# Kernel optimization log

Hardware: AMD Instinct MI355X
Metric: run time of the kernel (lower is better)

Reference implementation:

```python
import jax, jax.numpy as jnp
import numpy as np

HEADS = 16
DIM_HEAD = 64
QUERY_DIM = 1024
CONTEXT_DIM = 1024
D_ATTN = HEADS * DIM_HEAD
SCALE = DIM_HEAD ** -0.5


def setup_inputs() -> dict:
    key = jax.random.key(0)
    ks = jax.random.split(key, 7)
    B, N, M = 4, 2048, 1024
    x = jax.random.normal(ks[0], (B, N, QUERY_DIM), dtype=jnp.float32)
    context = jax.random.normal(ks[1], (B, M, CONTEXT_DIM), dtype=jnp.float32)
    # Linear weights stored as [in, out] (no bias for Q/K/V, bias for to_out)
    s = 0.02
    Wq = jax.random.normal(ks[2], (QUERY_DIM, D_ATTN), dtype=jnp.float32) * s
    Wk = jax.random.normal(ks[3], (CONTEXT_DIM, D_ATTN), dtype=jnp.float32) * s
    Wv = jax.random.normal(ks[4], (CONTEXT_DIM, D_ATTN), dtype=jnp.float32) * s
    Wo = jax.random.normal(ks[5], (D_ATTN, QUERY_DIM), dtype=jnp.float32) * s
    bo = jax.random.normal(ks[6], (QUERY_DIM,), dtype=jnp.float32) * s
    return {"x": x, "context": context, "Wq": Wq, "Wk": Wk, "Wv": Wv, "Wo": Wo, "bo": bo}


def reference(x, context, Wq, Wk, Wv, Wo, bo):
    B, N, _ = x.shape
    M = context.shape[1]
    Q = (x @ Wq).reshape(B, N, HEADS, DIM_HEAD)        # b n h d
    K = (context @ Wk).reshape(B, M, HEADS, DIM_HEAD)  # b m h d
    V = (context @ Wv).reshape(B, M, HEADS, DIM_HEAD)
    # scores: b q h m  (matches torch einsum 'bqhd,bhmd->bqhm')
    scores = jnp.einsum('bqhd,bmhd->bqhm', Q, K) * SCALE
    attn = jax.nn.softmax(scores, axis=-1)
    out = jnp.einsum('bqhm,bmhd->bqhd', attn, V)
    out = out.reshape(B, N, D_ATTN)
    return out @ Wo + bo  # dropout p=0.0 -> identity
```

## Files before the change

### kernel.cpp

```cpp
#include <hip/hip_runtime.h>
#include <math.h>


#define HEADS 16
#define DHEAD 64
#define DM    1024
#define BQ    4
#define NQ    2048
#define MK    1024

typedef unsigned short u16;
typedef __attribute__((ext_vector_type(8))) short bf16x8;
typedef __attribute__((ext_vector_type(4))) float f32x4;
typedef __attribute__((ext_vector_type(16))) float f32x16;

__device__ __forceinline__ u16 f2bf(float f) {
  unsigned u = __builtin_bit_cast(unsigned, f);
  u = u + 0x7FFFu + ((u >> 16) & 1u);
  return (u16)(u >> 16);
}

__device__ __forceinline__ unsigned cvtpk(float lo, float hi2) {
  unsigned r;
  asm("v_cvt_pk_bf16_f32 %0, %1, %2" : "=v"(r) : "v"(lo), "v"(hi2));
  return r;
}

__device__ __forceinline__ float max3f(float a, float b, float c) {
  float d;
  asm("v_max3_f32 %0, %1, %2, %3" : "=v"(d) : "v"(a), "v"(b), "v"(c));
  return d;
}

__device__ __forceinline__ void gld16(const u16* g, u16* l) {
  __builtin_amdgcn_global_load_lds((const __attribute__((address_space(1))) void*)g,
                                   (__attribute__((address_space(3))) void*)l,
                                   16, 0, 0);
}

__global__ void k_cvt(const float* __restrict__ in, u16* __restrict__ out, int n8) {
  int i = blockIdx.x * 256 + threadIdx.x;
  if (i >= n8) return;
  float4 a = ((const float4*)in)[i * 2];
  float4 b = ((const float4*)in)[i * 2 + 1];
  union { u16 h[8]; int4 v; } r;
  r.h[0] = f2bf(a.x); r.h[1] = f2bf(a.y); r.h[2] = f2bf(a.z); r.h[3] = f2bf(a.w);
  r.h[4] = f2bf(b.x); r.h[5] = f2bf(b.y); r.h[6] = f2bf(b.z); r.h[7] = f2bf(b.w);
  ((int4*)out)[i] = r.v;
}

__global__ void k_wt(const float* __restrict__ W0, const float* __restrict__ W1,
                     const float* __restrict__ W2, const float* __restrict__ W3,
                     u16* __restrict__ out) {
  __shared__ float t[32][33];
  const float* W = blockIdx.z == 0 ? W0 : blockIdx.z == 1 ? W1 : blockIdx.z == 2 ? W2 : W3;
  u16* o = out + (size_t)blockIdx.z * DM * DM;
  int r0 = blockIdx.y * 32, c0 = blockIdx.x * 32;
  int tx = threadIdx.x, ty = threadIdx.y;
  for (int i = ty; i < 32; i += 8) t[i][tx] = W[(size_t)(r0 + i) * DM + c0 + tx];
  __syncthreads();
  for (int i = ty; i < 32; i += 8) o[(size_t)(c0 + i) * DM + r0 + tx] = f2bf(t[tx][i]);
}


#define STG2(buf, k0) do {                               \
  gld16(gA0 + (k0), &As[buf][w * 512]);                  \
  gld16(gA1 + (k0), &As[buf][4096 + w * 512]);           \
  gld16(gB0 + (k0), &Bs[buf][w * 512]);                  \
} while (0)

#define GEMM2_COMPUTE(cur) do {                                                          \
  bf16x8 af[4], bfr[4];                                                                  \
  _Pragma("unroll")                                                                      \
  for (int mi = 0; mi < 4; mi++)                                                         \
    af[mi]  = *(const bf16x8*)&As[cur][(wr * 64 + mi * 16 + lrow) * 32 + sl];            \
  _Pragma("unroll")                                                                      \
  for (int ni = 0; ni < 4; ni++)                                                         \
    bfr[ni] = *(const bf16x8*)&Bs[cur][(wc * 64 + ni * 16 + lrow) * 32 + sl];            \
  __builtin_amdgcn_s_setprio(1);                                                         \
  _Pragma("unroll")                                                                      \
  for (int mi = 0; mi < 4; mi++)                                                         \
    _Pragma("unroll")                                                                    \
    for (int ni = 0; ni < 4; ni++)                                                       \
      acc[mi][ni] = __builtin_amdgcn_mfma_f32_16x16x32_bf16(af[mi], bfr[ni],             \
                                                            acc[mi][ni], 0, 0, 0);      \
  __builtin_amdgcn_s_setprio(0);                                                         \
} while (0)

#define GEMM2_LOOP() do {                                      \
  STG2(0, 0);                                                  \
  _Pragma("unroll 2")                                          \
  for (int kt = 0; kt < 32; ++kt) {                            \
    int cur = kt & 1;                                          \
    if (kt < 31) {                                             \
      STG2(cur ^ 1, (kt + 1) * 32);                            \
      asm volatile("s_waitcnt vmcnt(3)" ::: "memory");         \
    } else {                                                   \
      asm volatile("s_waitcnt vmcnt(0)" ::: "memory");         \
    }                                                          \
    __builtin_amdgcn_s_barrier();                              \
    __builtin_amdgcn_sched_barrier(0);                         \
    GEMM2_COMPUTE(cur);                                        \
    __builtin_amdgcn_sched_barrier(0);                         \
    __builtin_amdgcn_s_barrier();                              \
    __builtin_amdgcn_sched_barrier(0);                         \
  }                                                            \
} while (0)

__global__ __launch_bounds__(512, 2) void k_gemm_qkv(const u16* __restrict__ xb,
                                                     const u16* __restrict__ cb,
                                                     const u16* __restrict__ wt,
                                                     u16* __restrict__ Qb,
                                                     u16* __restrict__ Kb,
                                                     u16* __restrict__ Vtb) {
  __shared__ u16 As[2][8192];
  __shared__ u16 Bs[2][4096];
  int lin = blockIdx.x;
  int swz = (lin & 7) * 64 + (lin >> 3);
  int p = swz >> 3, bx = swz & 7;
  const u16* A; const u16* Bt; u16* obf; int row0, mode;
  if (p < 32)      { A = xb; Bt = wt;           obf = Qb;  row0 = p * 256;        mode = 0; }
  else if (p < 48) { A = cb; Bt = wt + 1048576; obf = Kb;  row0 = (p - 32) * 256; mode = 0; }
  else             { A = cb; Bt = wt + 2097152; obf = Vtb; row0 = (p - 48) * 256; mode = 1; }
  int col0 = bx * 128;
  int t = threadIdx.x;
  int w = t >> 6, lane = t & 63, lrow = lane & 15, lgrp = lane >> 4;
  int wr = w >> 1, wc = w & 1;
  int sl = (lgrp ^ (lrow & 3)) * 8;
  f32x4 acc[4][4] = {};
  int srow = t >> 2;
  int scol = ((t & 3) ^ (srow & 3)) * 8;
  const u16* gA0 = A  + (size_t)(row0 + srow) * DM + scol;
  const u16* gA1 = gA0 + (size_t)128 * DM;
  const u16* gB0 = Bt + (size_t)(col0 + srow) * DM + scol;

  GEMM2_LOOP();

  #pragma unroll
  for (int mi = 0; mi < 4; mi++)
    #pragma unroll
    for (int ni = 0; ni < 4; ni++)
      #pragma unroll
      for (int j = 0; j < 4; j++) {
        int gr = row0 + wr * 64 + mi * 16 + lgrp * 4 + j;
        int gc = col0 + wc * 64 + ni * 16 + lrow;
        float v = acc[mi][ni][j];
        if (mode == 0) {
          obf[(size_t)gr * DM + gc] = f2bf(v);
        } else {
          int b = gr >> 10, m = gr & 1023;
          obf[((size_t)(b * DM + gc)) * MK + m] = f2bf(v);
        }
      }
}

__global__ __launch_bounds__(512, 2) void k_gemm_o(const u16* __restrict__ A,
                                                   const u16* __restrict__ Bt,
                                                   float* __restrict__ of32,
                                                   const float* __restrict__ bias) {
  __shared__ u16 As[2][8192];
  __shared__ u16 Bs[2][4096];
  int lin = blockIdx.x;
  int swz = (lin & 7) * 32 + (lin >> 3);
  int p = swz >> 3, bx = swz & 7;
  int row0 = p * 256, col0 = bx * 128;
  int t = threadIdx.x;
  int w = t >> 6, lane = t & 63, lrow = lane & 15, lgrp = lane >> 4;
  int wr = w >> 1, wc = w & 1;
  int sl = (lgrp ^ (lrow & 3)) * 8;
  f32x4 acc[4][4] = {};
  int srow = t >> 2;
  int scol = ((t & 3) ^ (srow & 3)) * 8;
  const u16* gA0 = A  + (size_t)(row0 + srow) * DM + scol;
  const u16* gA1 = gA0 + (size_t)128 * DM;
  const u16* gB0 = Bt + (size_t)(col0 + srow) * DM + scol;

  GEMM2_LOOP();

  #pragma unroll
  for (int mi = 0; mi < 4; mi++)
    #pragma unroll
    for (int ni = 0; ni < 4; ni++)
      #pragma unroll
      for (int j = 0; j < 4; j++) {
        int gr = row0 + wr * 64 + mi * 16 + lgrp * 4 + j;
        int gc = col0 + wc * 64 + ni * 16 + lrow;
        of32[(size_t)gr * DM + gc] = acc[mi][ni][j] + bias[gc];
      }
}

#define BUILD_PFRAG(sv, base, frag) {                     \
  unsigned a_ = cvtpk(sv[base + 0], sv[base + 1]);        \
  unsigned c_ = cvtpk(sv[base + 2], sv[base + 3]);        \
  unsigned b_ = cvtpk(sv[base + 4], sv[base + 5]);        \
  unsigned d_ = cvtpk(sv[base + 6], sv[base + 7]);        \
  asm("v_permlane32_swap_b32 %0, %1" : "+v"(a_), "+v"(b_)); \
  asm("v_permlane32_swap_b32 %0, %1" : "+v"(c_), "+v"(d_)); \
  union { unsigned w[4]; bf16x8 v; } u_;                  \
  u_.w[0] = a_;  u_.w[1] = c_;                            \
  u_.w[2] = b_;  u_.w[3] = d_;                            \
  frag = u_.v; }

#define PV_CHUNK(sv, base, c) {                                               \
  bf16x8 pf_; BUILD_PFRAG(sv, base, pf_);                                     \
  int mo_ = ((c) * 16 + hi * 8) ^ sw;                                         \
  bf16x8 vf0_ = *(const bf16x8*)&Vlc[ln * 64 + mo_];                          \
  bf16x8 vf1_ = *(const bf16x8*)&Vlc[(32 + ln) * 64 + mo_];                   \
  __builtin_amdgcn_s_setprio(1);                                              \
  o0 = __builtin_amdgcn_mfma_f32_32x32x16_bf16(vf0_, pf_, o0, 0, 0, 0);       \
  o1 = __builtin_amdgcn_mfma_f32_32x32x16_bf16(vf1_, pf_, o1, 0, 0, 0);       \
  __builtin_amdgcn_s_setprio(0); }

__device__ __forceinline__ float max16(const f32x16 &v) {
  float m0 = max3f(v[0], v[1], v[2]);
  float m1 = max3f(v[3], v[4], v[5]);
  float m2 = max3f(v[6], v[7], v[8]);
  float m3 = max3f(v[9], v[10], v[11]);
  float m4 = max3f(v[12], v[13], v[14]);
  float a = max3f(m0, m1, m2);
  float b = max3f(m3, m4, v[15]);
  return fmaxf(a, b);
}

__device__ __forceinline__ float sum16(const f32x16 &v) {
  float a = (v[0] + v[1]) + (v[2] + v[3]);
  float b = (v[4] + v[5]) + (v[6] + v[7]);
  float c = (v[8] + v[9]) + (v[10] + v[11]);
  float d = (v[12] + v[13]) + (v[14] + v[15]);
  return (a + b) + (c + d);
}

__global__ __launch_bounds__(512) void k_attn(const u16* __restrict__ Q,
                                              const u16* __restrict__ K,
                                              const u16* __restrict__ Vt,
                                              u16* __restrict__ O) {
  __shared__ __align__(16) u16 Kl[2][4096];
  __shared__ __align__(16) u16 Vl[2][4096];
  int bh = blockIdx.y, b = bh >> 4, h = bh & 15;
  int n0 = blockIdx.x * 256;
  int t = threadIdx.x, w = t >> 6, lane = t & 63;
  int ln = lane & 31, hi = lane >> 5;
  const float s2 = 0.18033688011112042f;

  int qrow = n0 + w * 32 + ln;
  const u16* qp = &Q[(((size_t)(b * NQ + qrow)) * HEADS + h) * DHEAD + hi * 8];
  bf16x8 qf0 = *(const bf16x8*)(qp);
  bf16x8 qf1 = *(const bf16x8*)(qp + 16);
  bf16x8 qf2 = *(const bf16x8*)(qp + 32);
  bf16x8 qf3 = *(const bf16x8*)(qp + 48);

  f32x16 o0 = {}, o1 = {};
  float M_ = -1e30f, L_ = 0.f;

  int srow = t >> 3, sp = (t & 7) * 8;
  const u16* kg = &K[(((size_t)(b * MK + srow)) * HEADS + h) * DHEAD + sp];
  const u16* vg = &Vt[((size_t)(b * DM) + h * DHEAD + srow) * MK + sp];
  int sd = srow * 64 + (sp ^ ((srow & 7) << 3));
  int sw = (ln & 7) << 3;

  int4 kv = *(const int4*)kg;
  int4 vv = *(const int4*)vg;
  *(int4*)&Kl[0][sd] = kv;
  *(int4*)&Vl[0][sd] = vv;
  __syncthreads();

  for (int it = 0; it < 16; ++it) {
    int cur = it & 1;
    const u16* Klc = Kl[cur];
    const u16* Vlc = Vl[cur];
    if (it < 15) {
      kv = *(const int4*)(kg + (size_t)(it + 1) * (64 * HEADS * DHEAD));
      vv = *(const int4*)(vg + (it + 1) * 64);
    }

    f32x16 s0 = {}, s1 = {};
    __builtin_amdgcn_s_setprio(1);
    #pragma unroll
    for (int kd = 0; kd < 4; ++kd) {
      int doff = (kd * 16 + hi * 8) ^ sw;
      bf16x8 kf0 = *(const bf16x8*)&Klc[ln * 64 + doff];
      bf16x8 kf1 = *(const bf16x8*)&Klc[(32 + ln) * 64 + doff];
      bf16x8 qk = kd == 0 ? qf0 : kd == 1 ? qf1 : kd == 2 ? qf2 : qf3;
      s0 = __builtin_amdgcn_mfma_f32_32x32x16_bf16(kf0, qk, s0, 0, 0, 0);
      s1 = __builtin_amdgcn_mfma_f32_32x32x16_bf16(kf1, qk, s1, 0, 0, 0);
    }
    __builtin_amdgcn_s_setprio(0);

    float vm = fmaxf(max16(s0), max16(s1));

    if (!__all(vm - M_ <= 8.0f)) {
      float vm2 = fmaxf(vm, __shfl_xor(vm, 32));
      float mn = fmaxf(M_, vm2);
      float rc = exp2f((M_ - mn) * s2);
      M_ = mn;
      L_ *= rc;
      #pragma unroll
      for (int i = 0; i < 16; ++i) { o0[i] *= rc; o1[i] *= rc; }
    }
    float nb = M_ * s2;
    #pragma unroll
    for (int i = 0; i < 16; ++i) s0[i] = exp2f(s0[i] * s2 - nb);
    #pragma unroll
    for (int i = 0; i < 16; ++i) s1[i] = exp2f(s1[i] * s2 - nb);
    L_ += sum16(s0) + sum16(s1);

    PV_CHUNK(s0, 0, 0);
    PV_CHUNK(s0, 8, 1);
    PV_CHUNK(s1, 0, 2);
    PV_CHUNK(s1, 8, 3);

    if (it < 15) {
      *(int4*)&Kl[cur ^ 1][sd] = kv;
      *(int4*)&Vl[cur ^ 1][sd] = vv;
    }
    __syncthreads();
  }

  float Lt = L_ + __shfl_xor(L_, 32);
  float inv = 1.0f / Lt;
  u16* ob = (u16*)&O[(((size_t)(b * NQ + qrow)) * HEADS + h) * DHEAD];
  #pragma unroll
  for (int g = 0; g < 4; ++g) {
    union { u16 h4[4]; uint2 v; } r0, r1;
    #pragma unroll
    for (int s = 0; s < 4; ++s) {
      r0.h4[s] = f2bf(o0[4 * g + s] * inv);
      r1.h4[s] = f2bf(o1[4 * g + s] * inv);
    }
    *(uint2*)(ob + 8 * g + 4 * hi) = r0.v;
    *(uint2*)(ob + 32 + 8 * g + 4 * hi) = r1.v;
  }
}

extern "C" void kernel_launch(void* const* d_in, const int* in_sizes, int n_in,
                              void* d_out, int out_size, void* d_ws, size_t ws_size,
                              hipStream_t stream) {
  (void)in_sizes; (void)n_in; (void)out_size; (void)ws_size;
  const float* x   = (const float*)d_in[0];
  const float* ctx = (const float*)d_in[1];
  const float* Wq  = (const float*)d_in[2];
  const float* Wk  = (const float*)d_in[3];
  const float* Wv  = (const float*)d_in[4];
  const float* Wo  = (const float*)d_in[5];
  const float* bo  = (const float*)d_in[6];
  float* out = (float*)d_out;
  char* ws = (char*)d_ws;
  const size_t MB = 1u << 20;
  u16* xb  = (u16*)(ws);
  u16* cb  = (u16*)(ws + 16 * MB);
  u16* wt  = (u16*)(ws + 24 * MB);
  u16* Qb  = (u16*)(ws + 32 * MB);
  u16* Kb  = (u16*)(ws + 48 * MB);
  u16* Vtb = (u16*)(ws + 56 * MB);
  u16* Ab  = (u16*)(ws + 64 * MB);

  k_cvt<<<4096, 256, 0, stream>>>(x,   xb, 1048576);
  k_cvt<<<2048, 256, 0, stream>>>(ctx, cb, 524288);
  k_wt<<<dim3(32, 32, 4), dim3(32, 8), 0, stream>>>(Wq, Wk, Wv, Wo, wt);

  k_gemm_qkv<<<512, 512, 0, stream>>>(xb, cb, wt, Qb, Kb, Vtb);

  k_attn<<<dim3(8, 64), 512, 0, stream>>>(Qb, Kb, Vtb, Ab);

  k_gemm_o<<<256, 512, 0, stream>>>(Ab, wt + 3145728, out, bo);
}
```

Measured before the change: 175.6 us.

## Enlarge QKV GEMM tile to 256x256 with K=64 quadrant-phased pipeline

The QKV projection GEMM moves from 256x128 tiles with K=32 steps to 256x256 tiles with K=64 steps, using 16x16x32 MFMAs over four quadrant phases. Each phase reads its LDS fragments, issues the next global-to-LDS loads, and computes, giving finer-grained overlap of loads and math. The larger tile raises arithmetic intensity and halves the block count to 256. The cost is 64KB of LDS per block, which may limit occupancy, and more accumulator registers. The attention kernel's LDS pointer aliases are replaced by direct array indexing, a cosmetic change.

```diff
diff --git a/kernel.cpp b/kernel.cpp
--- a/kernel.cpp
+++ b/kernel.cpp
@@ -61,7 +61,6 @@
   __syncthreads();
   for (int i = ty; i < 32; i += 8) o[(size_t)(c0 + i) * DM + r0 + tx] = f2bf(t[tx][i]);
 }
-
 
 #define STG2(buf, k0) do {                               \
   gld16(gA0 + (k0), &As[buf][w * 512]);                  \
@@ -107,51 +106,128 @@
   }                                                            \
 } while (0)
 
+
+#define VM6 asm volatile("s_waitcnt vmcnt(6)" ::: "memory")
+
+#define STAGE_A8(bufi, h, kof) do {                                          \
+  gld16(gA + (size_t)(h) * 131072 + (kof), &As8[bufi][(h) * 8192 + w * 512]); \
+  gld16(gA + (size_t)(h) * 131072 + 65536 + (kof),                           \
+        &As8[bufi][(h) * 8192 + 4096 + w * 512]);                            \
+} while (0)
+
+#define STAGE_B8(bufi, h, kof) do {                                          \
+  gld16(gB + (size_t)(h) * 131072 + (kof), &Bs8[bufi][(h) * 8192 + w * 512]); \
+  gld16(gB + (size_t)(h) * 131072 + 65536 + (kof),                           \
+        &Bs8[bufi][(h) * 8192 + 4096 + w * 512]);                            \
+} while (0)
+
+#define RD_A8(qm) do { _Pragma("unroll")                                     \
+  for (int mi = 0; mi < 4; ++mi) {                                           \
+    const u16* pa = &As8[cur][((qm) * 128 + wmo + mi * 16 + lrow) * 64];     \
+    af8[mi][0] = *(const bf16x8*)(pa + fo0);                                 \
+    af8[mi][1] = *(const bf16x8*)(pa + (fo0 ^ 32));                          \
+  } } while (0)
+
+#define RD_B8(qn) do { _Pragma("unroll")                                     \
+  for (int ni = 0; ni < 2; ++ni) {                                           \
+    const u16* pb = &Bs8[cur][((qn) * 128 + wno + ni * 16 + lrow) * 64];     \
+    bf8[ni][0] = *(const bf16x8*)(pb + fo0);                                 \
+    bf8[ni][1] = *(const bf16x8*)(pb + (fo0 ^ 32));                          \
+  } } while (0)
+
+#define MM16(qm, qn) do {                                                    \
+  __builtin_amdgcn_s_setprio(1);                                             \
+  _Pragma("unroll")                                                          \
+  for (int mi = 0; mi < 4; ++mi)                                             \
+    _Pragma("unroll")                                                        \
+    for (int ni = 0; ni < 2; ++ni) {                                         \
+      acc[qm][qn][mi][ni] = __builtin_amdgcn_mfma_f32_16x16x32_bf16(         \
+          af8[mi][0], bf8[ni][0], acc[qm][qn][mi][ni], 0, 0, 0);             \
+      acc[qm][qn][mi][ni] = __builtin_amdgcn_mfma_f32_16x16x32_bf16(         \
+          af8[mi][1], bf8[ni][1], acc[qm][qn][mi][ni], 0, 0, 0);             \
+    }                                                                        \
+  __builtin_amdgcn_s_setprio(0);                                             \
+} while (0)
+
+#define PH8(RDS, STG, VM, qm, qn) do {                                       \
+  RDS;                                                                       \
+  __builtin_amdgcn_sched_barrier(0);                                         \
+  STG;                                                                       \
+  VM;                                                                        \
+  __builtin_amdgcn_s_barrier();                                              \
+  asm volatile("s_waitcnt lgkmcnt(0)" ::: "memory");                         \
+  __builtin_amdgcn_sched_barrier(0);                                         \
+  MM16(qm, qn);                                                              \
+  __builtin_amdgcn_sched_barrier(0);                                         \
+  __builtin_amdgcn_s_barrier();                                              \
+} while (0)
+
 __global__ __launch_bounds__(512, 2) void k_gemm_qkv(const u16* __restrict__ xb,
                                                      const u16* __restrict__ cb,
                                                      const u16* __restrict__ wt,
                                                      u16* __restrict__ Qb,
                                                      u16* __restrict__ Kb,
                                                      u16* __restrict__ Vtb) {
-  __shared__ u16 As[2][8192];
-  __shared__ u16 Bs[2][4096];
+  __shared__ u16 As8[2][16384];
+  __shared__ u16 Bs8[2][16384];
   int lin = blockIdx.x;
-  int swz = (lin & 7) * 64 + (lin >> 3);
-  int p = swz >> 3, bx = swz & 7;
+  int swz = (lin & 7) * 32 + (lin >> 3);
+  int p = swz >> 2, bx = swz & 3;
   const u16* A; const u16* Bt; u16* obf; int row0, mode;
   if (p < 32)      { A = xb; Bt = wt;           obf = Qb;  row0 = p * 256;        mode = 0; }
   else if (p < 48) { A = cb; Bt = wt + 1048576; obf = Kb;  row0 = (p - 32) * 256; mode = 0; }
   else             { A = cb; Bt = wt + 2097152; obf = Vtb; row0 = (p - 48) * 256; mode = 1; }
-  int col0 = bx * 128;
+  int col0 = bx * 256;
   int t = threadIdx.x;
   int w = t >> 6, lane = t & 63, lrow = lane & 15, lgrp = lane >> 4;
-  int wr = w >> 1, wc = w & 1;
-  int sl = (lgrp ^ (lrow & 3)) * 8;
-  f32x4 acc[4][4] = {};
-  int srow = t >> 2;
-  int scol = ((t & 3) ^ (srow & 3)) * 8;
-  const u16* gA0 = A  + (size_t)(row0 + srow) * DM + scol;
-  const u16* gA1 = gA0 + (size_t)128 * DM;
-  const u16* gB0 = Bt + (size_t)(col0 + srow) * DM + scol;
-
-  GEMM2_LOOP();
+  int wmo = (w >> 2) * 64, wno = (w & 3) * 32;
+  int fo0 = (lgrp ^ (lrow & 7)) * 8;
+  f32x4 acc[2][2][4][2] = {};
+  bf16x8 af8[4][2], bf8[2][2];
+  int srow = t >> 3, sunit = (t & 7) ^ ((t >> 3) & 7);
+  const u16* gA = A  + (size_t)(row0 + srow) * DM + sunit * 8;
+  const u16* gB = Bt + (size_t)(col0 + srow) * DM + sunit * 8;
+
+  STAGE_A8(0, 0, 0);
+  STAGE_B8(0, 1, 0);
+  STAGE_B8(0, 0, 0);
+  STAGE_A8(0, 1, 0);
+  STAGE_A8(1, 0, 64);
+  STAGE_B8(1, 1, 64);
+  VM6;
+  __syncthreads();
+
+  #pragma unroll 2
+  for (int u = 0; u < 16; ++u) {
+    int cur = u & 1, nxt = cur ^ 1;
+    int k1 = (u >= 15 ? 15 : u + 1) * 64;
+    int k2 = (u >= 14 ? 15 : u + 2) * 64;
+    PH8({ RD_A8(0); RD_B8(0); }, STAGE_B8(nxt, 0, k1), VM6,     0, 0);
+    PH8({ RD_B8(1); },           STAGE_A8(nxt, 1, k1), (void)0, 0, 1);
+    PH8({ RD_A8(1); },           STAGE_A8(cur, 0, k2), (void)0, 1, 1);
+    PH8({ RD_B8(0); },           STAGE_B8(cur, 1, k2), VM6,     1, 0);
+  }
 
   #pragma unroll
-  for (int mi = 0; mi < 4; mi++)
-    #pragma unroll
-    for (int ni = 0; ni < 4; ni++)
+  for (int qm = 0; qm < 2; ++qm)
+    #pragma unroll
+    for (int qn = 0; qn < 2; ++qn)
       #pragma unroll
-      for (int j = 0; j < 4; j++) {
-        int gr = row0 + wr * 64 + mi * 16 + lgrp * 4 + j;
-        int gc = col0 + wc * 64 + ni * 16 + lrow;
-        float v = acc[mi][ni][j];
-        if (mode == 0) {
-          obf[(size_t)gr * DM + gc] = f2bf(v);
-        } else {
-          int b = gr >> 10, m = gr & 1023;
-          obf[((size_t)(b * DM + gc)) * MK + m] = f2bf(v);
-        }
-      }
+      for (int mi = 0; mi < 4; ++mi)
+        #pragma unroll
+        for (int ni = 0; ni < 2; ++ni)
+          #pragma unroll
+          for (int j = 0; j < 4; ++j) {
+            int gr = row0 + qm * 128 + wmo + mi * 16 + lgrp * 4 + j;
+            int gc = col0 + qn * 128 + wno + ni * 16 + lrow;
+            float v = acc[qm][qn][mi][ni][j];
+            if (mode == 0) {
+              obf[(size_t)gr * DM + gc] = f2bf(v);
+            } else {
+              int b = gr >> 10, m = gr & 1023;
+              obf[((size_t)(b * DM + gc)) * MK + m] = f2bf(v);
+            }
+          }
 }
 
 __global__ __launch_bounds__(512, 2) void k_gemm_o(const u16* __restrict__ A,
@@ -204,8 +280,8 @@
 #define PV_CHUNK(sv, base, c) {                                               \
   bf16x8 pf_; BUILD_PFRAG(sv, base, pf_);                                     \
   int mo_ = ((c) * 16 + hi * 8) ^ sw;                                         \
-  bf16x8 vf0_ = *(const bf16x8*)&Vlc[ln * 64 + mo_];                          \
-  bf16x8 vf1_ = *(const bf16x8*)&Vlc[(32 + ln) * 64 + mo_];                   \
+  bf16x8 vf0_ = *(const bf16x8*)&Vl[cur][ln * 64 + mo_];                      \
+  bf16x8 vf1_ = *(const bf16x8*)&Vl[cur][(32 + ln) * 64 + mo_];               \
   __builtin_amdgcn_s_setprio(1);                                              \
   o0 = __builtin_amdgcn_mfma_f32_32x32x16_bf16(vf0_, pf_, o0, 0, 0, 0);       \
   o1 = __builtin_amdgcn_mfma_f32_32x32x16_bf16(vf1_, pf_, o1, 0, 0, 0);       \
@@ -266,8 +342,6 @@
 
   for (int it = 0; it < 16; ++it) {
     int cur = it & 1;
-    const u16* Klc = Kl[cur];
-    const u16* Vlc = Vl[cur];
     if (it < 15) {
       kv = *(const int4*)(kg + (size_t)(it + 1) * (64 * HEADS * DHEAD));
       vv = *(const int4*)(vg + (it + 1) * 64);
@@ -278,8 +352,8 @@
     #pragma unroll
     for (int kd = 0; kd < 4; ++kd) {
       int doff = (kd * 16 + hi * 8) ^ sw;
-      bf16x8 kf0 = *(const bf16x8*)&Klc[ln * 64 + doff];
-      bf16x8 kf1 = *(const bf16x8*)&Klc[(32 + ln) * 64 + doff];
+      bf16x8 kf0 = *(const bf16x8*)&Kl[cur][ln * 64 + doff];
+      bf16x8 kf1 = *(const bf16x8*)&Kl[cur][(32 + ln) * 64 + doff];
       bf16x8 qk = kd == 0 ? qf0 : kd == 1 ? qf1 : kd == 2 ? qf2 : qf3;
       s0 = __builtin_amdgcn_mfma_f32_32x32x16_bf16(kf0, qk, s0, 0, 0, 0);
       s1 = __builtin_amdgcn_mfma_f32_32x32x16_bf16(kf1, qk, s1, 0, 0, 0);
@@ -358,7 +432,7 @@
   k_cvt<<<2048, 256, 0, stream>>>(ctx, cb, 524288);
   k_wt<<<dim3(32, 32, 4), dim3(32, 8), 0, stream>>>(Wq, Wk, Wv, Wo, wt);
 
-  k_gemm_qkv<<<512, 512, 0, stream>>>(xb, cb, wt, Qb, Kb, Vtb);
+  k_gemm_qkv<<<256, 512, 0, stream>>>(xb, cb, wt, Qb, Kb, Vtb);
 
   k_attn<<<dim3(8, 64), 512, 0, stream>>>(Qb, Kb, Vtb, Ab);
 
```

Result: faster. 170.7 us (-2.8%).
